# Kernel optimization log

Hardware: AMD Instinct MI355X
Metric: run time of the kernel (lower is better)

The kernel has to match this reference:

```python
import jax, jax.numpy as jnp
import numpy as np

N_RAYS = 4096
N_SAMPLES = 256
K = 12           # K_samples stochastic draws
GRID = 160       # world_size per axis
K0_DIM = 12
PE = 4           # viewbase_pe
WIDTH = 128
BG_LEN = 0.2
XYZ_MIN = -1.0 - BG_LEN
XYZ_MAX = 1.0 + BG_LEN
ALPHA_INIT = 1e-4
ACT_SHIFT = float(np.log(1.0 / (1.0 - ALPHA_INIT) - 1.0))
VOXEL_SIZE = (XYZ_MAX - XYZ_MIN) / GRID
STEPDIST = 0.5 * VOXEL_SIZE
INTERVAL = 0.5   # stepsize * voxel_size_ratio
NEAR = 0.1


def setup_inputs() -> dict:
    key = jax.random.key(0)
    ks = jax.random.split(key, 12)
    dim0 = 3 + 3 * PE * 2 + K0_DIM  # 39
    return {
        'rays_o': jax.random.normal(ks[0], (N_RAYS, 3)) * 0.1,
        'rays_d': jax.random.normal(ks[1], (N_RAYS, 3)),
        'density_grid': jax.random.normal(ks[2], (1, GRID, GRID, GRID)) * 0.1,
        'density_std_grid': jnp.ones((1, GRID, GRID, GRID)) + 0.01 * jax.random.normal(ks[3], (1, GRID, GRID, GRID)),
        'k0_grid': jax.random.normal(ks[4], (K0_DIM, GRID, GRID, GRID)) * 0.1,
        'w0': jax.random.normal(ks[5], (dim0, WIDTH)) / np.sqrt(dim0),
        'b0': jnp.zeros((WIDTH,)),
        'w1': jax.random.normal(ks[6], (WIDTH, WIDTH)) / np.sqrt(WIDTH),
        'b1': jnp.zeros((WIDTH,)),
        'w2': jax.random.normal(ks[7], (WIDTH, 6)) / np.sqrt(WIDTH),
        'b2': jnp.zeros((6,)),
        'eps_den': jax.random.normal(ks[8], (K,)),
        'eps_rgb': jax.random.normal(ks[9], (K, 3)),
    }


def trilinear(grid, pts):
    # grid: [C, X, Y, Z]; pts: [..., 3] in world coords [XYZ_MIN, XYZ_MAX]
    # align_corners=True style index mapping (as torch grid_sample in DVGO)
    u = (pts - XYZ_MIN) / (XYZ_MAX - XYZ_MIN) * (GRID - 1)
    i0 = jnp.clip(jnp.floor(u), 0, GRID - 2).astype(jnp.int32)
    f = u - i0.astype(u.dtype)
    x0, y0, z0 = i0[..., 0], i0[..., 1], i0[..., 2]
    x1, y1, z1 = x0 + 1, y0 + 1, z0 + 1
    fx, fy, fz = f[..., 0], f[..., 1], f[..., 2]
    gx, gy, gz = 1.0 - fx, 1.0 - fy, 1.0 - fz
    out = (grid[:, x0, y0, z0] * (gx * gy * gz)
         + grid[:, x1, y0, z0] * (fx * gy * gz)
         + grid[:, x0, y1, z0] * (gx * fy * gz)
         + grid[:, x0, y0, z1] * (gx * gy * fz)
         + grid[:, x1, y1, z0] * (fx * fy * gz)
         + grid[:, x1, y0, z1] * (fx * gy * fz)
         + grid[:, x0, y1, z1] * (gx * fy * fz)
         + grid[:, x1, y1, z1] * (fx * fy * fz))  # [C, ...]
    return jnp.moveaxis(out, 0, -1)


def _forward(rays_o, rays_d, density_grid, density_std_grid, k0_grid,
             w0, b0, w1, b1, w2, b2, eps_den, eps_rgb):
    viewdirs = rays_d / jnp.linalg.norm(rays_d, axis=-1, keepdims=True)  # [N,3]
    t = NEAR + STEPDIST * jnp.arange(N_SAMPLES, dtype=rays_o.dtype)      # [S]
    pts = rays_o[:, None, :] + viewdirs[:, None, :] * t[None, :, None]   # [N,S,3]

    # inf-norm scene contraction (contracted_norm='inf')
    norm = jnp.max(jnp.abs(pts), axis=-1, keepdims=True)
    inner = norm <= 1.0
    pts_c = jnp.where(inner, pts, pts / norm * ((1.0 + BG_LEN) - BG_LEN / norm))

    raw_den = trilinear(density_grid, pts_c)[..., 0]              # [N,S]
    raw_std = trilinear(density_std_grid, pts_c)[..., 0]          # [N,S]
    std = jax.nn.softplus(raw_std)
    # stochastic density draws: [N,S,K]
    den_k = raw_den[..., None] + std[..., None] * eps_den[None, None, :]
    alpha = 1.0 - jnp.exp(-jax.nn.softplus(den_k + ACT_SHIFT) * INTERVAL)
    # exclusive cumprod transmittance along samples
    T = jnp.cumprod(1.0 - alpha + 1e-10, axis=1)
    T = jnp.concatenate([jnp.ones_like(T[:, :1]), T[:, :-1]], axis=1)
    weights = alpha * T                                            # [N,S,K]

    # shading: k0 features + view PE -> rgbnet MLP -> 6 (rgb mean, rgb std)
    k0 = trilinear(k0_grid, pts_c)                                 # [N,S,12]
    freq = (2.0 ** jnp.arange(PE, dtype=pts.dtype))
    vd = viewdirs[:, :, None] * freq[None, None, :]                # [N,3,PE]
    vemb = jnp.concatenate([viewdirs, jnp.sin(vd).reshape(-1, 3 * PE),
                            jnp.cos(vd).reshape(-1, 3 * PE)], axis=-1)  # [N,27]
    feat = jnp.concatenate([k0, jnp.broadcast_to(vemb[:, None, :], (k0.shape[0], k0.shape[1], vemb.shape[-1]))], axis=-1)  # [N,S,39]
    h = jax.nn.relu(feat @ w0 + b0)
    h = jax.nn.relu(h @ w1 + b1)
    out6 = h @ w2 + b2                                             # [N,S,6]
    rgb_mean, rgb_raw_std = out6[..., :3], out6[..., 3:]
    rgb_std = jax.nn.softplus(rgb_raw_std)
    # stochastic rgb draws: [N,S,K,3]
    rgb_k = jax.nn.sigmoid(rgb_mean[:, :, None, :] + rgb_std[:, :, None, :] * eps_rgb[None, None, :, :])

    rgb_marched = jnp.sum(weights[..., None] * rgb_k, axis=1)      # [N,K,3]
    acc = jnp.sum(weights, axis=1)                                 # [N,K]
    rgb_marched = rgb_marched + (1.0 - acc)[..., None]             # white bg
    return jnp.mean(rgb_marched, axis=1)                           # [N,3]


def reference(rays_o, rays_d, density_grid, density_std_grid, k0_grid,
              w0, b0, w1, b1, w2, b2, eps_den, eps_rgb):
    return _forward(rays_o, rays_d, density_grid, density_std_grid, k0_grid,
                    w0, b0, w1, b1, w2, b2, eps_den, eps_rgb)
```

## Files before the change

kernel.cpp:

```cpp
#include <hip/hip_runtime.h>
#include <hip/hip_bf16.h>
#include <math.h>

#define NRAYS 4096
#define KK    12
#define GS    160
#define G3    (GS*GS*GS)
#define NSAMP (NRAYS*256)

typedef __bf16 bf16x8 __attribute__((ext_vector_type(8)));
typedef float  f32x4  __attribute__((ext_vector_type(4)));

#define W0KT_OFF 0
#define W1T_OFF  4096
#define W2T_OFF  20480
#define GRID_OFF_B 65536
#define FEAT_OFF_B 131137536UL
#define WKA_OFF_B  164691968UL
#define WKB_OFF_B  181469184UL
#define NEED_SPLIT 189857792UL
#define NEED_GRID  131137536UL

__device__ __forceinline__ float softplusf(float x) {
    return fmaxf(x, 0.f) + log1pf(expf(-fabsf(x)));
}
__device__ __forceinline__ float sigmoidf(float x) {
    return 1.f / (1.f + __expf(-x));
}
__device__ __forceinline__ unsigned pk2(float a, float b) {
    unsigned short x = __builtin_bit_cast(unsigned short, (__bf16)a);
    unsigned short y = __builtin_bit_cast(unsigned short, (__bf16)b);
    return (unsigned)x | ((unsigned)y << 16);
}
__device__ __forceinline__ float bfw(unsigned u, int hi) {
    return __builtin_bit_cast(float, hi ? (u & 0xffff0000u) : (u << 16));
}
__device__ __forceinline__ int xoff(int m, int kb) {
    return m * 256 + (kb ^ ((m & 7) << 4));
}

__global__ void prep_weights(const float* __restrict__ w0, const float* __restrict__ w1,
                             const float* __restrict__ w2, __bf16* __restrict__ ws)
{
    int i = blockIdx.x * 256 + threadIdx.x;
    if (i < 4096) {
        int n = i >> 5, k = i & 31;
        ws[W0KT_OFF + i] = (__bf16)((k < 12) ? w0[k * 128 + n] : 0.f);
    } else if (i < 20480) {
        int j = i - 4096;
        int n = j >> 7, k = j & 127;
        ws[W1T_OFF + j] = (__bf16)(w1[k * 128 + n]);
    } else if (i < 22528) {
        int j = i - 20480;
        int n = j >> 7, k = j & 127;
        ws[W2T_OFF + j] = (__bf16)((n < 6) ? w2[k * 6 + n] : 0.f);
    }
}

__global__ void prep_grid(const float* __restrict__ dg, const float* __restrict__ sg,
                          const float* __restrict__ k0, __bf16* __restrict__ dst)
{
    int v = blockIdx.x * 256 + threadIdx.x;
    float vals[16];
    vals[0] = dg[v];
    vals[1] = sg[v];
#pragma unroll
    for (int c = 0; c < 12; ++c) vals[2 + c] = k0[c * G3 + v];
    vals[14] = 0.f; vals[15] = 0.f;
    uint4 o0, o1;
    o0.x = pk2(vals[0],  vals[1]);  o0.y = pk2(vals[2],  vals[3]);
    o0.z = pk2(vals[4],  vals[5]);  o0.w = pk2(vals[6],  vals[7]);
    o1.x = pk2(vals[8],  vals[9]);  o1.y = pk2(vals[10], vals[11]);
    o1.z = pk2(vals[12], vals[13]); o1.w = pk2(vals[14], vals[15]);
    uint4* p = (uint4*)(dst + (size_t)v * 16);
    p[0] = o0; p[1] = o1;
}

__global__ __launch_bounds__(256, 2)
void voxgo_gather(const float* __restrict__ rays_o, const float* __restrict__ rays_d,
                  const char* __restrict__ gridb, const float* __restrict__ eps_den,
                  uint4* __restrict__ feat, uint4* __restrict__ wk_a,
                  uint2* __restrict__ wk_b)
{
    const float BGL   = 0.2f;
    const float XMIN  = -1.2f;
    const float SCALE = 159.0f / 2.4f;
    const float ACT_SHIFT = -9.2102403672f;
    const float STEP  = 0.0075f;
    const float NEART = 0.1f;

    __shared__ float scanw[4][KK];

    const int r    = blockIdx.x;
    const int s    = threadIdx.x;
    const int lane = s & 63;
    const int wv   = s >> 6;

    float dx = rays_d[r*3+0], dy = rays_d[r*3+1], dz = rays_d[r*3+2];
    float inv = rsqrtf(dx*dx + dy*dy + dz*dz);
    dx *= inv; dy *= inv; dz *= inv;
    float t  = NEART + STEP * (float)s;
    float px = rays_o[r*3+0] + dx*t;
    float py = rays_o[r*3+1] + dy*t;
    float pz = rays_o[r*3+2] + dz*t;
    float an = fmaxf(fabsf(px), fmaxf(fabsf(py), fabsf(pz)));
    if (an > 1.0f) {
        float sc = (1.0f + BGL - BGL/an) / an;
        px *= sc; py *= sc; pz *= sc;
    }
    float ux = (px - XMIN)*SCALE, uy = (py - XMIN)*SCALE, uz = (pz - XMIN)*SCALE;
    int ix = min(max((int)floorf(ux), 0), GS-2);
    int iy = min(max((int)floorf(uy), 0), GS-2);
    int iz = min(max((int)floorf(uz), 0), GS-2);
    float fx = ux-(float)ix, fy = uy-(float)iy, fz = uz-(float)iz;
    float gx = 1.f-fx, gy = 1.f-fy, gz = 1.f-fz;
    const int o000 = (ix*GS + iy)*GS + iz;
    float c00 = gx*gy, c01 = gx*fy, c10 = fx*gy, c11 = fx*fy;

    float acc14[14];
#pragma unroll
    for (int c = 0; c < 14; ++c) acc14[c] = 0.f;
    const int   vi[4] = { o000, o000 + GS, o000 + GS*GS, o000 + GS*GS + GS };
    const float cw[4] = { c00, c01, c10, c11 };
#pragma unroll
    for (int p = 0; p < 4; ++p) {
        const uint4* vp = (const uint4*)(gridb + (size_t)vi[p] * 32);
        uint4 q0 = vp[0], q1 = vp[1], q2 = vp[2], q3 = vp[3];
        float wz0 = cw[p]*gz, wz1 = cw[p]*fz;
        unsigned z0w[8] = { q0.x, q0.y, q0.z, q0.w, q1.x, q1.y, q1.z, q1.w };
        unsigned z1w[8] = { q2.x, q2.y, q2.z, q2.w, q3.x, q3.y, q3.z, q3.w };
#pragma unroll
        for (int c = 0; c < 14; ++c) {
            float a = bfw(z0w[c >> 1], c & 1);
            float b = bfw(z1w[c >> 1], c & 1);
            acc14[c] = fmaf(wz0, a, fmaf(wz1, b, acc14[c]));
        }
    }
    float raw_den = acc14[0];
    float raw_std = acc14[1];

    float stdv = softplusf(raw_std);
    float alpha[KK], incl[KK];
#pragma unroll
    for (int k = 0; k < KK; ++k) {
        float x  = raw_den + stdv * eps_den[k] + ACT_SHIFT;
        float a  = __expf(x) * 0.5f;
        float al = a - a*a*0.5f;
        alpha[k] = al;
        incl[k]  = 1.f - al + 1e-10f;
    }
#pragma unroll
    for (int d = 1; d < 64; d <<= 1) {
#pragma unroll
        for (int k = 0; k < KK; ++k) {
            float v = __shfl_up(incl[k], d, 64);
            if (lane >= d) incl[k] *= v;
        }
    }
    if (lane == 63) {
#pragma unroll
        for (int k = 0; k < KK; ++k) scanw[wv][k] = incl[k];
    }
    __syncthreads();
    float wk[KK];
#pragma unroll
    for (int k = 0; k < KK; ++k) {
        float pref = 1.f;
        for (int pw = 0; pw < wv; ++pw) pref *= scanw[pw][k];
        float ex = __shfl_up(incl[k], 1, 64);
        if (lane == 0) ex = 1.f;
        wk[k] = alpha[k] * (pref * ex);
    }

    const int rid = r * 256 + s;
    uint4 q0, q1;
    q0.x = pk2(acc14[2], acc14[3]);  q0.y = pk2(acc14[4],  acc14[5]);
    q0.z = pk2(acc14[6], acc14[7]);  q0.w = pk2(acc14[8],  acc14[9]);
    q1.x = pk2(acc14[10], acc14[11]); q1.y = pk2(acc14[12], acc14[13]);
    q1.z = 0u; q1.w = 0u;
    feat[(size_t)rid*2 + 0] = q0;
    feat[(size_t)rid*2 + 1] = q1;
    uint4 wa; uint2 wb;
    wa.x = pk2(wk[0], wk[1]); wa.y = pk2(wk[2], wk[3]);
    wa.z = pk2(wk[4], wk[5]); wa.w = pk2(wk[6], wk[7]);
    wb.x = pk2(wk[8], wk[9]); wb.y = pk2(wk[10], wk[11]);
    wk_a[rid] = wa;
    wk_b[rid] = wb;
}

__global__ __launch_bounds__(512, 2)
void voxgo_mlp(const float* __restrict__ rays_d,
               const float* __restrict__ w0, const float* __restrict__ b0,
               const float* __restrict__ b1, const float* __restrict__ b2,
               const float* __restrict__ eps_rgb,
               const __bf16* __restrict__ wsb,
               const uint4* __restrict__ feat, const uint4* __restrict__ wk_a,
               const uint2* __restrict__ wk_b,
               float* __restrict__ out)
{
    __shared__ char  xb[65536];
    __shared__ float h1ray[128];
    __shared__ float veb[27];
    __shared__ float red[8][3];

    const int r    = blockIdx.x;
    const int t    = threadIdx.x;
    const int lane = t & 63;
    const int wv   = t >> 6;
    const int lm = lane & 15, lk = lane >> 4;
    const int Mb = wv * 32;

    float dx = rays_d[r*3+0], dy = rays_d[r*3+1], dz = rays_d[r*3+2];
    float inv = rsqrtf(dx*dx + dy*dy + dz*dz);
    dx *= inv; dy *= inv; dz *= inv;
    if (t < 27) {
        float v;
        if (t < 3)       v = (t == 0) ? dx : (t == 1) ? dy : dz;
        else {
            int j = (t - 3) % 12;
            int a = j >> 2, p = j & 3;
            float arg = ((a == 0) ? dx : (a == 1) ? dy : dz) * (float)(1 << p);
            float sv, cv;
            __sincosf(arg, &sv, &cv);
            v = (t < 15) ? sv : cv;
        }
        veb[t] = v;
    }
    __syncthreads();
    if (t < 128) {
        float acc = b0[t];
#pragma unroll
        for (int j = 0; j < 27; ++j)
            acc = fmaf(veb[j], w0[(12 + j) * 128 + t], acc);
        h1ray[t] = acc;
    }
    __syncthreads();

    f32x4 acc[2][8];
#pragma unroll
    for (int nt = 0; nt < 8; ++nt) {
        f32x4 bi = *(const f32x4*)(h1ray + nt*16 + lk*4);
        acc[0][nt] = bi; acc[1][nt] = bi;
    }
    {
        const __bf16* w0t = wsb + W0KT_OFF;
        const uint4* fb = feat + (size_t)r * 512;
        bf16x8 bfr[2];
#pragma unroll
        for (int mt = 0; mt < 2; ++mt) {
            uint4 fq = {0u, 0u, 0u, 0u};
            if (lk < 2) fq = fb[(Mb + mt*16 + lm)*2 + lk];
            bfr[mt] = __builtin_bit_cast(bf16x8, fq);
        }
#pragma unroll
        for (int nt = 0; nt < 8; ++nt) {
            bf16x8 af = *(const bf16x8*)(w0t + (nt*16 + lm)*32 + lk*8);
#pragma unroll
            for (int mt = 0; mt < 2; ++mt)
                acc[mt][nt] = __builtin_amdgcn_mfma_f32_16x16x32_bf16(af, bfr[mt], acc[mt][nt], 0, 0, 0);
        }
    }
#pragma unroll
    for (int mt = 0; mt < 2; ++mt) {
        int mr = Mb + mt*16 + lm;
#pragma unroll
        for (int nt = 0; nt < 8; ++nt) {
            f32x4 v = acc[mt][nt];
            uint2 p;
            p.x = pk2(fmaxf(v.x, 0.f), fmaxf(v.y, 0.f));
            p.y = pk2(fmaxf(v.z, 0.f), fmaxf(v.w, 0.f));
            *(uint2*)(xb + xoff(mr, nt*32 + lk*8)) = p;
        }
    }
#pragma unroll
    for (int nt = 0; nt < 8; ++nt) {
        int n0 = nt*16 + lk*4;
        f32x4 bi = { b1[n0], b1[n0+1], b1[n0+2], b1[n0+3] };
        acc[0][nt] = bi; acc[1][nt] = bi;
    }
    {
        const __bf16* w1t = wsb + W1T_OFF;
#pragma unroll
        for (int ks = 0; ks < 4; ++ks) {
            bf16x8 bfr[2];
#pragma unroll
            for (int mt = 0; mt < 2; ++mt)
                bfr[mt] = *(const bf16x8*)(xb + xoff(Mb + mt*16 + lm, ks*64 + lk*16));
#pragma unroll
            for (int nt = 0; nt < 8; ++nt) {
                bf16x8 af = *(const bf16x8*)(w1t + (nt*16 + lm)*128 + ks*32 + lk*8);
#pragma unroll
                for (int mt = 0; mt < 2; ++mt)
                    acc[mt][nt] = __builtin_amdgcn_mfma_f32_16x16x32_bf16(af, bfr[mt], acc[mt][nt], 0, 0, 0);
            }
        }
    }
#pragma unroll
    for (int mt = 0; mt < 2; ++mt) {
        int mr = Mb + mt*16 + lm;
#pragma unroll
        for (int nt = 0; nt < 8; ++nt) {
            f32x4 v = acc[mt][nt];
            uint2 p;
            p.x = pk2(fmaxf(v.x, 0.f), fmaxf(v.y, 0.f));
            p.y = pk2(fmaxf(v.z, 0.f), fmaxf(v.w, 0.f));
            *(uint2*)(xb + xoff(mr, nt*32 + lk*8)) = p;
        }
    }
    f32x4 a3[2];
    {
        const __bf16* w2t = wsb + W2T_OFF;
        f32x4 bi;
        bi.x = (lk*4+0 < 6) ? b2[lk*4+0] : 0.f;
        bi.y = (lk*4+1 < 6) ? b2[lk*4+1] : 0.f;
        bi.z = (lk*4+2 < 6) ? b2[lk*4+2] : 0.f;
        bi.w = (lk*4+3 < 6) ? b2[lk*4+3] : 0.f;
        a3[0] = bi; a3[1] = bi;
#pragma unroll
        for (int ks = 0; ks < 4; ++ks) {
            bf16x8 af = *(const bf16x8*)(w2t + lm*128 + ks*32 + lk*8);
#pragma unroll
            for (int mt = 0; mt < 2; ++mt) {
                bf16x8 bfr = *(const bf16x8*)(xb + xoff(Mb + mt*16 + lm, ks*64 + lk*16));
                a3[mt] = __builtin_amdgcn_mfma_f32_16x16x32_bf16(af, bfr, a3[mt], 0, 0, 0);
            }
        }
    }
    {
        char* o6b = xb + wv * 8192;
#pragma unroll
        for (int mt = 0; mt < 2; ++mt)
            *(f32x4*)(o6b + (mt*16 + lm)*80 + lk*16) = a3[mt];
    }
    __syncthreads();

    float p0 = 0.f, p1 = 0.f, p2 = 0.f;
    {
        const int sm  = t & 255;
        const int hf  = t >> 8;
        const float* orow = (const float*)(xb + (sm >> 5) * 8192 + (sm & 31) * 80);
        float m0 = orow[0], m1 = orow[1], m2 = orow[2];
        float s0 = softplusf(orow[3]), s1 = softplusf(orow[4]), s2 = softplusf(orow[5]);
        const int rid = r * 256 + sm;
        uint4 wa = wk_a[rid];
        float w6[6];
        if (hf == 0) {
            w6[0] = bfw(wa.x, 0); w6[1] = bfw(wa.x, 1); w6[2] = bfw(wa.y, 0);
            w6[3] = bfw(wa.y, 1); w6[4] = bfw(wa.z, 0); w6[5] = bfw(wa.z, 1);
        } else {
            uint2 wb = wk_b[rid];
            w6[0] = bfw(wa.w, 0); w6[1] = bfw(wa.w, 1); w6[2] = bfw(wb.x, 0);
            w6[3] = bfw(wb.x, 1); w6[4] = bfw(wb.y, 0); w6[5] = bfw(wb.y, 1);
        }
        const int kb = hf * 6;
#pragma unroll
        for (int kk = 0; kk < 6; ++kk) {
            int k = kb + kk;
            float w = w6[kk];
            p0 += w * (sigmoidf(m0 + s0*eps_rgb[k*3+0]) - 1.f);
            p1 += w * (sigmoidf(m1 + s1*eps_rgb[k*3+1]) - 1.f);
            p2 += w * (sigmoidf(m2 + s2*eps_rgb[k*3+2]) - 1.f);
        }
    }
#pragma unroll
    for (int d = 32; d > 0; d >>= 1) {
        p0 += __shfl_down(p0, d, 64);
        p1 += __shfl_down(p1, d, 64);
        p2 += __shfl_down(p2, d, 64);
    }
    if (lane == 0) { red[wv][0] = p0; red[wv][1] = p1; red[wv][2] = p2; }
    __syncthreads();
    if (t == 0) {
        float a0 = 0.f, a1 = 0.f, a2 = 0.f;
#pragma unroll
        for (int w = 0; w < 8; ++w) { a0 += red[w][0]; a1 += red[w][1]; a2 += red[w][2]; }
        out[r*3+0] = 1.f + a0 * (1.f/12.f);
        out[r*3+1] = 1.f + a1 * (1.f/12.f);
        out[r*3+2] = 1.f + a2 * (1.f/12.f);
    }
}

template<int ITL>
__global__ __launch_bounds__(256, 2)
void voxgo_fwd(const float* __restrict__ rays_o, const float* __restrict__ rays_d,
               const float* __restrict__ dgrid, const float* __restrict__ sgrid,
               const float* __restrict__ k0g, const char* __restrict__ gridb,
               const float* __restrict__ w0, const float* __restrict__ b0,
               const float* __restrict__ b1, const float* __restrict__ b2,
               const float* __restrict__ eps_den, const float* __restrict__ eps_rgb,
               const __bf16* __restrict__ wsb,
               float* __restrict__ out)
{
    const float BGL   = 0.2f;
    const float XMIN  = -1.2f;
    const float SCALE = 159.0f / 2.4f;
    const float ACT_SHIFT = -9.2102403672f;
    const float STEP  = 0.0075f;
    const float NEART = 0.1f;

    __shared__ char  xb[65536];
    __shared__ float h1ray[128];
    __shared__ float veb[27];
    __shared__ float scanw[4][KK];
    __shared__ float red[4][3];

    const int r    = blockIdx.x;
    const int s    = threadIdx.x;
    const int lane = s & 63;
    const int wv   = s >> 6;
    const int lm = lane & 15, lk = lane >> 4;
    const int Mb = wv * 64;

    float dx = rays_d[r*3+0], dy = rays_d[r*3+1], dz = rays_d[r*3+2];
    float inv = rsqrtf(dx*dx + dy*dy + dz*dz);
    dx *= inv; dy *= inv; dz *= inv;
    if (s < 27) {
        float v;
        if (s < 3)       v = (s == 0) ? dx : (s == 1) ? dy : dz;
        else {
            int j = (s - 3) % 12;
            int a = j >> 2, p = j & 3;
            float arg = ((a == 0) ? dx : (a == 1) ? dy : dz) * (float)(1 << p);
            float sv, cv;
            __sincosf(arg, &sv, &cv);
            v = (s < 15) ? sv : cv;
        }
        veb[s] = v;
    }
    float t  = NEART + STEP * (float)s;
    float px = rays_o[r*3+0] + dx*t;
    float py = rays_o[r*3+1] + dy*t;
    float pz = rays_o[r*3+2] + dz*t;
    float an = fmaxf(fabsf(px), fmaxf(fabsf(py), fabsf(pz)));
    if (an > 1.0f) {
        float sc = (1.0f + BGL - BGL/an) / an;
        px *= sc; py *= sc; pz *= sc;
    }
    float ux = (px - XMIN)*SCALE, uy = (py - XMIN)*SCALE, uz = (pz - XMIN)*SCALE;
    int ix = min(max((int)floorf(ux), 0), GS-2);
    int iy = min(max((int)floorf(uy), 0), GS-2);
    int iz = min(max((int)floorf(uz), 0), GS-2);
    float fx = ux-(float)ix, fy = uy-(float)iy, fz = uz-(float)iz;
    float gx = 1.f-fx, gy = 1.f-fy, gz = 1.f-fz;
    const int o000 = (ix*GS + iy)*GS + iz;
    float c00 = gx*gy, c01 = gx*fy, c10 = fx*gy, c11 = fx*fy;

    float raw_den, raw_std, k0v[KK];
    if constexpr (ITL) {
        float acc14[14];
#pragma unroll
        for (int c = 0; c < 14; ++c) acc14[c] = 0.f;
        const int   vi[4] = { o000, o000 + GS, o000 + GS*GS, o000 + GS*GS + GS };
        const float cw[4] = { c00, c01, c10, c11 };
#pragma unroll
        for (int p = 0; p < 4; ++p) {
            const uint4* vp = (const uint4*)(gridb + (size_t)vi[p] * 32);
            uint4 q0 = vp[0], q1 = vp[1], q2 = vp[2], q3 = vp[3];
            float wz0 = cw[p]*gz, wz1 = cw[p]*fz;
            unsigned z0w[8] = { q0.x, q0.y, q0.z, q0.w, q1.x, q1.y, q1.z, q1.w };
            unsigned z1w[8] = { q2.x, q2.y, q2.z, q2.w, q3.x, q3.y, q3.z, q3.w };
#pragma unroll
            for (int c = 0; c < 14; ++c) {
                float a = bfw(z0w[c >> 1], c & 1);
                float b = bfw(z1w[c >> 1], c & 1);
                acc14[c] = fmaf(wz0, a, fmaf(wz1, b, acc14[c]));
            }
        }
        raw_den = acc14[0];
        raw_std = acc14[1];
#pragma unroll
        for (int c = 0; c < KK; ++c) k0v[c] = acc14[2 + c];
    } else {
        const int oY = GS, oX = GS*GS;
        auto tri = [&](const float* __restrict__ g) -> float {
            float v00 = g[o000]*gz       + g[o000+1]*fz;
            float v01 = g[o000+oY]*gz    + g[o000+oY+1]*fz;
            float v10 = g[o000+oX]*gz    + g[o000+oX+1]*fz;
            float v11 = g[o000+oX+oY]*gz + g[o000+oX+oY+1]*fz;
            return v00*c00 + v01*c01 + v10*c10 + v11*c11;
        };
        raw_den = tri(dgrid);
        raw_std = tri(sgrid);
#pragma unroll
        for (int c = 0; c < KK; ++c) k0v[c] = tri(k0g + c*G3);
    }

    float stdv = softplusf(raw_std);
    float alpha[KK], incl[KK];
#pragma unroll
    for (int k = 0; k < KK; ++k) {
        float x  = raw_den + stdv * eps_den[k] + ACT_SHIFT;
        float a  = __expf(x) * 0.5f;
        float al = a - a*a*0.5f;
        alpha[k] = al;
        incl[k]  = 1.f - al + 1e-10f;
    }
#pragma unroll
    for (int d = 1; d < 64; d <<= 1) {
#pragma unroll
        for (int k = 0; k < KK; ++k) {
            float v = __shfl_up(incl[k], d, 64);
            if (lane >= d) incl[k] *= v;
        }
    }
    if (lane == 63) {
#pragma unroll
        for (int k = 0; k < KK; ++k) scanw[wv][k] = incl[k];
    }
    {
        uint4 v;
        v.x = pk2(k0v[0], k0v[1]); v.y = pk2(k0v[2],  k0v[3]);
        v.z = pk2(k0v[4], k0v[5]); v.w = pk2(k0v[6],  k0v[7]);
        *(uint4*)(xb + xoff(s, 0)) = v;
        v.x = pk2(k0v[8], k0v[9]); v.y = pk2(k0v[10], k0v[11]);
        v.z = 0u; v.w = 0u;
        *(uint4*)(xb + xoff(s, 16)) = v;
        uint4 z4 = {0u, 0u, 0u, 0u};
        *(uint4*)(xb + xoff(s, 32)) = z4;
        *(uint4*)(xb + xoff(s, 48)) = z4;
    }
    __syncthreads();
    float wk[KK];
#pragma unroll
    for (int k = 0; k < KK; ++k) {
        float pref = 1.f;
        for (int pw = 0; pw < wv; ++pw) pref *= scanw[pw][k];
        float ex = __shfl_up(incl[k], 1, 64);
        if (lane == 0) ex = 1.f;
        wk[k] = alpha[k] * (pref * ex);
    }
    if (s < 128) {
        float acc = b0[s];
#pragma unroll
        for (int j = 0; j < 27; ++j)
            acc = fmaf(veb[j], w0[(12 + j) * 128 + s], acc);
        h1ray[s] = acc;
    }
    __syncthreads();

    f32x4 acc[4][8];
#pragma unroll
    for (int nt = 0; nt < 8; ++nt) {
        f32x4 bi = *(const f32x4*)(h1ray + nt*16 + lk*4);
#pragma unroll
        for (int mt = 0; mt < 4; ++mt) acc[mt][nt] = bi;
    }
    {
        const __bf16* w0t = wsb + W0KT_OFF;
        bf16x8 bfr[4];
#pragma unroll
        for (int mt = 0; mt < 4; ++mt)
            bfr[mt] = *(const bf16x8*)(xb + xoff(Mb + mt*16 + lm, lk*16));
#pragma unroll
        for (int nt = 0; nt < 8; ++nt) {
            bf16x8 af = *(const bf16x8*)(w0t + (nt*16 + lm)*32 + lk*8);
#pragma unroll
            for (int mt = 0; mt < 4; ++mt)
                acc[mt][nt] = __builtin_amdgcn_mfma_f32_16x16x32_bf16(af, bfr[mt], acc[mt][nt], 0, 0, 0);
        }
    }
#pragma unroll
    for (int mt = 0; mt < 4; ++mt) {
        int mr = Mb + mt*16 + lm;
#pragma unroll
        for (int nt = 0; nt < 8; ++nt) {
            f32x4 v = acc[mt][nt];
            uint2 p;
            p.x = pk2(fmaxf(v.x, 0.f), fmaxf(v.y, 0.f));
            p.y = pk2(fmaxf(v.z, 0.f), fmaxf(v.w, 0.f));
            *(uint2*)(xb + xoff(mr, nt*32 + lk*8)) = p;
        }
    }
#pragma unroll
    for (int nt = 0; nt < 8; ++nt) {
        int n0 = nt*16 + lk*4;
        f32x4 bi = { b1[n0], b1[n0+1], b1[n0+2], b1[n0+3] };
#pragma unroll
        for (int mt = 0; mt < 4; ++mt) acc[mt][nt] = bi;
    }
    {
        const __bf16* w1t = wsb + W1T_OFF;
#pragma unroll
        for (int ks = 0; ks < 4; ++ks) {
            bf16x8 bfr[4];
#pragma unroll
            for (int mt = 0; mt < 4; ++mt)
                bfr[mt] = *(const bf16x8*)(xb + xoff(Mb + mt*16 + lm, ks*64 + lk*16));
#pragma unroll
            for (int nt = 0; nt < 8; ++nt) {
                bf16x8 af = *(const bf16x8*)(w1t + (nt*16 + lm)*128 + ks*32 + lk*8);
#pragma unroll
                for (int mt = 0; mt < 4; ++mt)
                    acc[mt][nt] = __builtin_amdgcn_mfma_f32_16x16x32_bf16(af, bfr[mt], acc[mt][nt], 0, 0, 0);
            }
        }
    }
#pragma unroll
    for (int mt = 0; mt < 4; ++mt) {
        int mr = Mb + mt*16 + lm;
#pragma unroll
        for (int nt = 0; nt < 8; ++nt) {
            f32x4 v = acc[mt][nt];
            uint2 p;
            p.x = pk2(fmaxf(v.x, 0.f), fmaxf(v.y, 0.f));
            p.y = pk2(fmaxf(v.z, 0.f), fmaxf(v.w, 0.f));
            *(uint2*)(xb + xoff(mr, nt*32 + lk*8)) = p;
        }
    }
    f32x4 a3[4];
    {
        const __bf16* w2t = wsb + W2T_OFF;
        f32x4 bi;
        bi.x = (lk*4+0 < 6) ? b2[lk*4+0] : 0.f;
        bi.y = (lk*4+1 < 6) ? b2[lk*4+1] : 0.f;
        bi.z = (lk*4+2 < 6) ? b2[lk*4+2] : 0.f;
        bi.w = (lk*4+3 < 6) ? b2[lk*4+3] : 0.f;
#pragma unroll
        for (int mt = 0; mt < 4; ++mt) a3[mt] = bi;
#pragma unroll
        for (int ks = 0; ks < 4; ++ks) {
            bf16x8 af = *(const bf16x8*)(w2t + lm*128 + ks*32 + lk*8);
#pragma unroll
            for (int mt = 0; mt < 4; ++mt) {
                bf16x8 bfr = *(const bf16x8*)(xb + xoff(Mb + mt*16 + lm, ks*64 + lk*16));
                a3[mt] = __builtin_amdgcn_mfma_f32_16x16x32_bf16(af, bfr, a3[mt], 0, 0, 0);
            }
        }
    }
    {
        char* o6b = xb + wv * 16384;
#pragma unroll
        for (int mt = 0; mt < 4; ++mt)
            *(f32x4*)(o6b + (mt*16 + lm)*80 + lk*16) = a3[mt];
    }
    float p0 = 0.f, p1 = 0.f, p2 = 0.f;
    {
        const float* orow = (const float*)(xb + wv*16384 + lane*80);
        float m0 = orow[0], m1 = orow[1], m2 = orow[2];
        float s0 = softplusf(orow[3]), s1 = softplusf(orow[4]), s2 = softplusf(orow[5]);
#pragma unroll
        for (int k = 0; k < KK; ++k) {
            float w = wk[k];
            p0 += w * (sigmoidf(m0 + s0*eps_rgb[k*3+0]) - 1.f);
            p1 += w * (sigmoidf(m1 + s1*eps_rgb[k*3+1]) - 1.f);
            p2 += w * (sigmoidf(m2 + s2*eps_rgb[k*3+2]) - 1.f);
        }
    }
#pragma unroll
    for (int d = 32; d > 0; d >>= 1) {
        p0 += __shfl_down(p0, d, 64);
        p1 += __shfl_down(p1, d, 64);
        p2 += __shfl_down(p2, d, 64);
    }
    if (lane == 0) { red[wv][0] = p0; red[wv][1] = p1; red[wv][2] = p2; }
    __syncthreads();
    if (s == 0) {
        float a0 = red[0][0] + red[1][0] + red[2][0] + red[3][0];
        float a1 = red[0][1] + red[1][1] + red[2][1] + red[3][1];
        float a2 = red[0][2] + red[1][2] + red[2][2] + red[3][2];
        out[r*3+0] = 1.f + a0 * (1.f/12.f);
        out[r*3+1] = 1.f + a1 * (1.f/12.f);
        out[r*3+2] = 1.f + a2 * (1.f/12.f);
    }
}

extern "C" void kernel_launch(void* const* d_in, const int* in_sizes, int n_in,
                              void* d_out, int out_size, void* d_ws, size_t ws_size,
                              hipStream_t stream) {
    const float* rays_o  = (const float*)d_in[0];
    const float* rays_d  = (const float*)d_in[1];
    const float* dgrid   = (const float*)d_in[2];
    const float* sgrid   = (const float*)d_in[3];
    const float* k0g     = (const float*)d_in[4];
    const float* w0      = (const float*)d_in[5];
    const float* b0      = (const float*)d_in[6];
    const float* w1      = (const float*)d_in[7];
    const float* b1      = (const float*)d_in[8];
    const float* w2      = (const float*)d_in[9];
    const float* b2      = (const float*)d_in[10];
    const float* eps_den = (const float*)d_in[11];
    const float* eps_rgb = (const float*)d_in[12];
    float* out = (float*)d_out;
    __bf16* wsb = (__bf16*)d_ws;
    char*   base  = (char*)d_ws;
    char*   gridb = base + GRID_OFF_B;

    prep_weights<<<88, 256, 0, stream>>>(w0, w1, w2, wsb);
    if (ws_size >= NEED_SPLIT) {
        prep_grid<<<G3/256, 256, 0, stream>>>(dgrid, sgrid, k0g, (__bf16*)gridb);
        uint4* feat = (uint4*)(base + FEAT_OFF_B);
        uint4* wk_a = (uint4*)(base + WKA_OFF_B);
        uint2* wk_b = (uint2*)(base + WKB_OFF_B);
        voxgo_gather<<<NRAYS, 256, 0, stream>>>(rays_o, rays_d, gridb, eps_den,
                                                feat, wk_a, wk_b);
        voxgo_mlp<<<NRAYS, 512, 0, stream>>>(rays_d, w0, b0, b1, b2, eps_rgb,
                                             wsb, feat, wk_a, wk_b, out);
    } else if (ws_size >= NEED_GRID) {
        prep_grid<<<G3/256, 256, 0, stream>>>(dgrid, sgrid, k0g, (__bf16*)gridb);
        voxgo_fwd<1><<<NRAYS, 256, 0, stream>>>(rays_o, rays_d, dgrid, sgrid, k0g, gridb,
                                                w0, b0, b1, b2, eps_den, eps_rgb, wsb, out);
    } else {
        voxgo_fwd<0><<<NRAYS, 256, 0, stream>>>(rays_o, rays_d, dgrid, sgrid, k0g, gridb,
                                                w0, b0, b1, b2, eps_den, eps_rgb, wsb, out);
    }
}
```

Baseline: 299.4 us.

## Split MLP kernel into four 64-sample blocks per ray with LDS-staged weights

Result: slower. 323.6 us (+8.1%).

```diff
diff --git a/kernel.cpp b/kernel.cpp
--- a/kernel.cpp
+++ b/kernel.cpp
@@ -80,7 +80,7 @@
 void voxgo_gather(const float* __restrict__ rays_o, const float* __restrict__ rays_d,
                   const char* __restrict__ gridb, const float* __restrict__ eps_den,
                   uint4* __restrict__ feat, uint4* __restrict__ wk_a,
-                  uint2* __restrict__ wk_b)
+                  uint2* __restrict__ wk_b, float* __restrict__ out)
 {
     const float BGL   = 0.2f;
     const float XMIN  = -1.2f;
@@ -95,6 +95,8 @@
     const int s    = threadIdx.x;
     const int lane = s & 63;
     const int wv   = s >> 6;
+
+    if (s < 3) out[r*3 + s] = 1.0f;
 
     float dx = rays_d[r*3+0], dy = rays_d[r*3+1], dz = rays_d[r*3+2];
     float inv = rsqrtf(dx*dx + dy*dy + dz*dz);
@@ -188,7 +190,7 @@
     wk_b[rid] = wb;
 }
 
-__global__ __launch_bounds__(512, 2)
+__global__ __launch_bounds__(256, 2)
 void voxgo_mlp(const float* __restrict__ rays_d,
                const float* __restrict__ w0, const float* __restrict__ b0,
                const float* __restrict__ b1, const float* __restrict__ b2,
@@ -198,165 +200,152 @@
                const uint2* __restrict__ wk_b,
                float* __restrict__ out)
 {
-    __shared__ char  xb[65536];
-    __shared__ float h1ray[128];
-    __shared__ float veb[27];
-    __shared__ float red[8][3];
-
-    const int r    = blockIdx.x;
-    const int t    = threadIdx.x;
-    const int lane = t & 63;
-    const int wv   = t >> 6;
+    __shared__ char   wl[32768];
+    __shared__ __bf16 w0l[128*32];
+    __shared__ __bf16 w2l[16*128];
+    __shared__ char   act[64*256];
+    __shared__ float  h1ray[128];
+    __shared__ float  veb[32];
+    __shared__ float  red[4][4];
+
+    const int blk  = blockIdx.x;
+    const int r    = blk >> 2;
+    const int q    = blk & 3;
+    const int s    = threadIdx.x;
+    const int lane = s & 63;
+    const int wv   = s >> 6;
     const int lm = lane & 15, lk = lane >> 4;
-    const int Mb = wv * 32;
+    const int Mb = wv * 16;
+
+    {
+        const uint4* g1 = (const uint4*)(wsb + W1T_OFF);
+#pragma unroll
+        for (int j = 0; j < 8; ++j) {
+            int i = j * 256 + s;
+            *(uint4*)(wl + xoff(i >> 4, (i & 15) << 4)) = g1[i];
+        }
+        const uint4* g0 = (const uint4*)(wsb + W0KT_OFF);
+        ((uint4*)w0l)[s]       = g0[s];
+        ((uint4*)w0l)[s + 256] = g0[s + 256];
+        const uint4* g2 = (const uint4*)(wsb + W2T_OFF);
+        ((uint4*)w2l)[s] = g2[s];
+    }
 
     float dx = rays_d[r*3+0], dy = rays_d[r*3+1], dz = rays_d[r*3+2];
     float inv = rsqrtf(dx*dx + dy*dy + dz*dz);
     dx *= inv; dy *= inv; dz *= inv;
-    if (t < 27) {
+    if (s < 27) {
         float v;
-        if (t < 3)       v = (t == 0) ? dx : (t == 1) ? dy : dz;
+        if (s < 3)       v = (s == 0) ? dx : (s == 1) ? dy : dz;
         else {
-            int j = (t - 3) % 12;
+            int j = (s - 3) % 12;
             int a = j >> 2, p = j & 3;
             float arg = ((a == 0) ? dx : (a == 1) ? dy : dz) * (float)(1 << p);
             float sv, cv;
             __sincosf(arg, &sv, &cv);
-            v = (t < 15) ? sv : cv;
-        }
-        veb[t] = v;
-    }
-    __syncthreads();
-    if (t < 128) {
-        float acc = b0[t];
+            v = (s < 15) ? sv : cv;
+        }
+        veb[s] = v;
+    }
+
+    {
+        const int row  = s >> 2;
+        const int part = s & 3;
+        const size_t rid = (size_t)r * 256 + q * 64 + row;
+        uint4 v = {0u, 0u, 0u, 0u};
+        if (part < 2) v = feat[rid * 2 + part];
+        *(uint4*)(act + xoff(row, part * 16)) = v;
+    }
+    __syncthreads();
+
+    if (s < 128) {
+        float acc = b0[s];
 #pragma unroll
         for (int j = 0; j < 27; ++j)
-            acc = fmaf(veb[j], w0[(12 + j) * 128 + t], acc);
-        h1ray[t] = acc;
-    }
-    __syncthreads();
-
-    f32x4 acc[2][8];
+            acc = fmaf(veb[j], w0[(12 + j) * 128 + s], acc);
+        h1ray[s] = acc;
+    }
+    __syncthreads();
+
+    f32x4 acc[8];
+#pragma unroll
+    for (int nt = 0; nt < 8; ++nt)
+        acc[nt] = *(const f32x4*)(h1ray + nt*16 + lk*4);
+    {
+        bf16x8 bfr = *(const bf16x8*)(act + xoff(Mb + lm, lk*16));
+#pragma unroll
+        for (int nt = 0; nt < 8; ++nt) {
+            bf16x8 af = *(const bf16x8*)(w0l + (nt*16 + lm)*32 + lk*8);
+            acc[nt] = __builtin_amdgcn_mfma_f32_16x16x32_bf16(af, bfr, acc[nt], 0, 0, 0);
+        }
+    }
 #pragma unroll
     for (int nt = 0; nt < 8; ++nt) {
-        f32x4 bi = *(const f32x4*)(h1ray + nt*16 + lk*4);
-        acc[0][nt] = bi; acc[1][nt] = bi;
-    }
-    {
-        const __bf16* w0t = wsb + W0KT_OFF;
-        const uint4* fb = feat + (size_t)r * 512;
-        bf16x8 bfr[2];
-#pragma unroll
-        for (int mt = 0; mt < 2; ++mt) {
-            uint4 fq = {0u, 0u, 0u, 0u};
-            if (lk < 2) fq = fb[(Mb + mt*16 + lm)*2 + lk];
-            bfr[mt] = __builtin_bit_cast(bf16x8, fq);
-        }
-#pragma unroll
-        for (int nt = 0; nt < 8; ++nt) {
-            bf16x8 af = *(const bf16x8*)(w0t + (nt*16 + lm)*32 + lk*8);
-#pragma unroll
-            for (int mt = 0; mt < 2; ++mt)
-                acc[mt][nt] = __builtin_amdgcn_mfma_f32_16x16x32_bf16(af, bfr[mt], acc[mt][nt], 0, 0, 0);
-        }
-    }
-#pragma unroll
-    for (int mt = 0; mt < 2; ++mt) {
-        int mr = Mb + mt*16 + lm;
-#pragma unroll
-        for (int nt = 0; nt < 8; ++nt) {
-            f32x4 v = acc[mt][nt];
-            uint2 p;
-            p.x = pk2(fmaxf(v.x, 0.f), fmaxf(v.y, 0.f));
-            p.y = pk2(fmaxf(v.z, 0.f), fmaxf(v.w, 0.f));
-            *(uint2*)(xb + xoff(mr, nt*32 + lk*8)) = p;
-        }
+        f32x4 v = acc[nt];
+        uint2 p;
+        p.x = pk2(fmaxf(v.x, 0.f), fmaxf(v.y, 0.f));
+        p.y = pk2(fmaxf(v.z, 0.f), fmaxf(v.w, 0.f));
+        *(uint2*)(act + xoff(Mb + lm, nt*32 + lk*8)) = p;
     }
 #pragma unroll
     for (int nt = 0; nt < 8; ++nt) {
         int n0 = nt*16 + lk*4;
         f32x4 bi = { b1[n0], b1[n0+1], b1[n0+2], b1[n0+3] };
-        acc[0][nt] = bi; acc[1][nt] = bi;
-    }
-    {
-        const __bf16* w1t = wsb + W1T_OFF;
-#pragma unroll
-        for (int ks = 0; ks < 4; ++ks) {
-            bf16x8 bfr[2];
-#pragma unroll
-            for (int mt = 0; mt < 2; ++mt)
-                bfr[mt] = *(const bf16x8*)(xb + xoff(Mb + mt*16 + lm, ks*64 + lk*16));
-#pragma unroll
-            for (int nt = 0; nt < 8; ++nt) {
-                bf16x8 af = *(const bf16x8*)(w1t + (nt*16 + lm)*128 + ks*32 + lk*8);
-#pragma unroll
-                for (int mt = 0; mt < 2; ++mt)
-                    acc[mt][nt] = __builtin_amdgcn_mfma_f32_16x16x32_bf16(af, bfr[mt], acc[mt][nt], 0, 0, 0);
-            }
-        }
-    }
-#pragma unroll
-    for (int mt = 0; mt < 2; ++mt) {
-        int mr = Mb + mt*16 + lm;
+        acc[nt] = bi;
+    }
+#pragma unroll
+    for (int ks = 0; ks < 4; ++ks) {
+        bf16x8 bfr = *(const bf16x8*)(act + xoff(Mb + lm, ks*64 + lk*16));
 #pragma unroll
         for (int nt = 0; nt < 8; ++nt) {
-            f32x4 v = acc[mt][nt];
-            uint2 p;
-            p.x = pk2(fmaxf(v.x, 0.f), fmaxf(v.y, 0.f));
-            p.y = pk2(fmaxf(v.z, 0.f), fmaxf(v.w, 0.f));
-            *(uint2*)(xb + xoff(mr, nt*32 + lk*8)) = p;
-        }
-    }
-    f32x4 a3[2];
-    {
-        const __bf16* w2t = wsb + W2T_OFF;
-        f32x4 bi;
-        bi.x = (lk*4+0 < 6) ? b2[lk*4+0] : 0.f;
-        bi.y = (lk*4+1 < 6) ? b2[lk*4+1] : 0.f;
-        bi.z = (lk*4+2 < 6) ? b2[lk*4+2] : 0.f;
-        bi.w = (lk*4+3 < 6) ? b2[lk*4+3] : 0.f;
-        a3[0] = bi; a3[1] = bi;
-#pragma unroll
-        for (int ks = 0; ks < 4; ++ks) {
-            bf16x8 af = *(const bf16x8*)(w2t + lm*128 + ks*32 + lk*8);
-#pragma unroll
-            for (int mt = 0; mt < 2; ++mt) {
-                bf16x8 bfr = *(const bf16x8*)(xb + xoff(Mb + mt*16 + lm, ks*64 + lk*16));
-                a3[mt] = __builtin_amdgcn_mfma_f32_16x16x32_bf16(af, bfr, a3[mt], 0, 0, 0);
-            }
-        }
-    }
-    {
-        char* o6b = xb + wv * 8192;
-#pragma unroll
-        for (int mt = 0; mt < 2; ++mt)
-            *(f32x4*)(o6b + (mt*16 + lm)*80 + lk*16) = a3[mt];
-    }
+            bf16x8 af = *(const bf16x8*)(wl + xoff(nt*16 + lm, ks*64 + lk*16));
+            acc[nt] = __builtin_amdgcn_mfma_f32_16x16x32_bf16(af, bfr, acc[nt], 0, 0, 0);
+        }
+    }
+#pragma unroll
+    for (int nt = 0; nt < 8; ++nt) {
+        f32x4 v = acc[nt];
+        uint2 p;
+        p.x = pk2(fmaxf(v.x, 0.f), fmaxf(v.y, 0.f));
+        p.y = pk2(fmaxf(v.z, 0.f), fmaxf(v.w, 0.f));
+        *(uint2*)(act + xoff(Mb + lm, nt*32 + lk*8)) = p;
+    }
+    f32x4 a3;
+    a3.x = (lk*4+0 < 6) ? b2[lk*4+0] : 0.f;
+    a3.y = (lk*4+1 < 6) ? b2[lk*4+1] : 0.f;
+    a3.z = (lk*4+2 < 6) ? b2[lk*4+2] : 0.f;
+    a3.w = (lk*4+3 < 6) ? b2[lk*4+3] : 0.f;
+#pragma unroll
+    for (int ks = 0; ks < 4; ++ks) {
+        bf16x8 af  = *(const bf16x8*)(w2l + lm*128 + ks*32 + lk*8);
+        bf16x8 bfr = *(const bf16x8*)(act + xoff(Mb + lm, ks*64 + lk*16));
+        a3 = __builtin_amdgcn_mfma_f32_16x16x32_bf16(af, bfr, a3, 0, 0, 0);
+    }
+    *(f32x4*)(act + wv*4096 + lm*80 + lk*16) = a3;
     __syncthreads();
 
     float p0 = 0.f, p1 = 0.f, p2 = 0.f;
     {
-        const int sm  = t & 255;
-        const int hf  = t >> 8;
-        const float* orow = (const float*)(xb + (sm >> 5) * 8192 + (sm & 31) * 80);
+        const int row  = s & 63;
+        const int part = s >> 6;
+        const float* orow = (const float*)(act + (row >> 4)*4096 + (row & 15)*80);
         float m0 = orow[0], m1 = orow[1], m2 = orow[2];
         float s0 = softplusf(orow[3]), s1 = softplusf(orow[4]), s2 = softplusf(orow[5]);
-        const int rid = r * 256 + sm;
+        const size_t rid = (size_t)r * 256 + q * 64 + row;
         uint4 wa = wk_a[rid];
-        float w6[6];
-        if (hf == 0) {
-            w6[0] = bfw(wa.x, 0); w6[1] = bfw(wa.x, 1); w6[2] = bfw(wa.y, 0);
-            w6[3] = bfw(wa.y, 1); w6[4] = bfw(wa.z, 0); w6[5] = bfw(wa.z, 1);
-        } else {
-            uint2 wb = wk_b[rid];
-            w6[0] = bfw(wa.w, 0); w6[1] = bfw(wa.w, 1); w6[2] = bfw(wb.x, 0);
-            w6[3] = bfw(wb.x, 1); w6[4] = bfw(wb.y, 0); w6[5] = bfw(wb.y, 1);
-        }
-        const int kb = hf * 6;
-#pragma unroll
-        for (int kk = 0; kk < 6; ++kk) {
+        uint2 wb = wk_b[rid];
+        float wv0 = (part==0) ? bfw(wa.x,0) : (part==1) ? bfw(wa.y,1)
+                  : (part==2) ? bfw(wa.w,0) : bfw(wb.x,1);
+        float wv1 = (part==0) ? bfw(wa.x,1) : (part==1) ? bfw(wa.z,0)
+                  : (part==2) ? bfw(wa.w,1) : bfw(wb.y,0);
+        float wv2 = (part==0) ? bfw(wa.y,0) : (part==1) ? bfw(wa.z,1)
+                  : (part==2) ? bfw(wb.x,0) : bfw(wb.y,1);
+        float w3[3] = { wv0, wv1, wv2 };
+        const int kb = part * 3;
+#pragma unroll
+        for (int kk = 0; kk < 3; ++kk) {
             int k = kb + kk;
-            float w = w6[kk];
+            float w = w3[kk];
             p0 += w * (sigmoidf(m0 + s0*eps_rgb[k*3+0]) - 1.f);
             p1 += w * (sigmoidf(m1 + s1*eps_rgb[k*3+1]) - 1.f);
             p2 += w * (sigmoidf(m2 + s2*eps_rgb[k*3+2]) - 1.f);
@@ -370,13 +359,13 @@
     }
     if (lane == 0) { red[wv][0] = p0; red[wv][1] = p1; red[wv][2] = p2; }
     __syncthreads();
-    if (t == 0) {
-        float a0 = 0.f, a1 = 0.f, a2 = 0.f;
-#pragma unroll
-        for (int w = 0; w < 8; ++w) { a0 += red[w][0]; a1 += red[w][1]; a2 += red[w][2]; }
-        out[r*3+0] = 1.f + a0 * (1.f/12.f);
-        out[r*3+1] = 1.f + a1 * (1.f/12.f);
-        out[r*3+2] = 1.f + a2 * (1.f/12.f);
+    if (s == 0) {
+        float a0 = red[0][0] + red[1][0] + red[2][0] + red[3][0];
+        float a1 = red[0][1] + red[1][1] + red[2][1] + red[3][1];
+        float a2 = red[0][2] + red[1][2] + red[2][2] + red[3][2];
+        atomicAdd(&out[r*3+0], a0 * (1.f/12.f));
+        atomicAdd(&out[r*3+1], a1 * (1.f/12.f));
+        atomicAdd(&out[r*3+2], a2 * (1.f/12.f));
     }
 }
 
@@ -692,9 +681,9 @@
         uint4* wk_a = (uint4*)(base + WKA_OFF_B);
         uint2* wk_b = (uint2*)(base + WKB_OFF_B);
         voxgo_gather<<<NRAYS, 256, 0, stream>>>(rays_o, rays_d, gridb, eps_den,
-                                                feat, wk_a, wk_b);
-        voxgo_mlp<<<NRAYS, 512, 0, stream>>>(rays_d, w0, b0, b1, b2, eps_rgb,
-                                             wsb, feat, wk_a, wk_b, out);
+                                                feat, wk_a, wk_b, out);
+        voxgo_mlp<<<NRAYS*4, 256, 0, stream>>>(rays_d, w0, b0, b1, b2, eps_rgb,
+                                               wsb, feat, wk_a, wk_b, out);
     } else if (ws_size >= NEED_GRID) {
         prep_grid<<<G3/256, 256, 0, stream>>>(dgrid, sgrid, k0g, (__bf16*)gridb);
         voxgo_fwd<1><<<NRAYS, 256, 0, stream>>>(rays_o, rays_d, dgrid, sgrid, k0g, gridb,
```

## Split MLP kernel into half-ray blocks with LDS-staged features and atomic output

Applied to the files above, without the earlier changes.

Result: faster. 290.9 us (-2.9%).

```diff
diff --git a/kernel.cpp b/kernel.cpp
--- a/kernel.cpp
+++ b/kernel.cpp
@@ -22,7 +22,7 @@
 #define NEED_GRID  131137536UL
 
 __device__ __forceinline__ float softplusf(float x) {
-    return fmaxf(x, 0.f) + log1pf(expf(-fabsf(x)));
+    return fmaxf(x, 0.f) + __logf(1.f + __expf(-fabsf(x)));
 }
 __device__ __forceinline__ float sigmoidf(float x) {
     return 1.f / (1.f + __expf(-x));
@@ -80,7 +80,7 @@
 void voxgo_gather(const float* __restrict__ rays_o, const float* __restrict__ rays_d,
                   const char* __restrict__ gridb, const float* __restrict__ eps_den,
                   uint4* __restrict__ feat, uint4* __restrict__ wk_a,
-                  uint2* __restrict__ wk_b)
+                  uint2* __restrict__ wk_b, float* __restrict__ out)
 {
     const float BGL   = 0.2f;
     const float XMIN  = -1.2f;
@@ -95,6 +95,8 @@
     const int s    = threadIdx.x;
     const int lane = s & 63;
     const int wv   = s >> 6;
+
+    if (s < 3) out[r*3 + s] = 1.0f;
 
     float dx = rays_d[r*3+0], dy = rays_d[r*3+1], dz = rays_d[r*3+2];
     float inv = rsqrtf(dx*dx + dy*dy + dz*dz);
@@ -188,7 +190,7 @@
     wk_b[rid] = wb;
 }
 
-__global__ __launch_bounds__(512, 2)
+__global__ __launch_bounds__(256, 2)
 void voxgo_mlp(const float* __restrict__ rays_d,
                const float* __restrict__ w0, const float* __restrict__ b0,
                const float* __restrict__ b1, const float* __restrict__ b2,
@@ -198,41 +200,54 @@
                const uint2* __restrict__ wk_b,
                float* __restrict__ out)
 {
-    __shared__ char  xb[65536];
+    __shared__ char  act[128 * 256];
     __shared__ float h1ray[128];
-    __shared__ float veb[27];
-    __shared__ float red[8][3];
-
-    const int r    = blockIdx.x;
-    const int t    = threadIdx.x;
-    const int lane = t & 63;
-    const int wv   = t >> 6;
+    __shared__ float veb[32];
+    __shared__ float red[4][4];
+
+    const int blk  = blockIdx.x;
+    const int r    = blk >> 1;
+    const int hlf  = blk & 1;
+    const int s    = threadIdx.x;
+    const int lane = s & 63;
+    const int wv   = s >> 6;
     const int lm = lane & 15, lk = lane >> 4;
     const int Mb = wv * 32;
 
     float dx = rays_d[r*3+0], dy = rays_d[r*3+1], dz = rays_d[r*3+2];
     float inv = rsqrtf(dx*dx + dy*dy + dz*dz);
     dx *= inv; dy *= inv; dz *= inv;
-    if (t < 27) {
+    if (s < 27) {
         float v;
-        if (t < 3)       v = (t == 0) ? dx : (t == 1) ? dy : dz;
+        if (s < 3)       v = (s == 0) ? dx : (s == 1) ? dy : dz;
         else {
-            int j = (t - 3) % 12;
+            int j = (s - 3) % 12;
             int a = j >> 2, p = j & 3;
             float arg = ((a == 0) ? dx : (a == 1) ? dy : dz) * (float)(1 << p);
             float sv, cv;
             __sincosf(arg, &sv, &cv);
-            v = (t < 15) ? sv : cv;
-        }
-        veb[t] = v;
+            v = (s < 15) ? sv : cv;
+        }
+        veb[s] = v;
+    }
+
+    {
+        const int row  = s >> 1;
+        const int part = s & 1;
+        const size_t rid = (size_t)r * 256 + hlf * 128 + row;
+        uint4 v = feat[rid * 2 + part];
+        *(uint4*)(act + xoff(row, part * 16)) = v;
+        uint4 z4 = {0u, 0u, 0u, 0u};
+        *(uint4*)(act + xoff(row, 32 + part * 16)) = z4;
     }
     __syncthreads();
-    if (t < 128) {
-        float acc = b0[t];
+
+    if (s < 128) {
+        float acc = b0[s];
 #pragma unroll
         for (int j = 0; j < 27; ++j)
-            acc = fmaf(veb[j], w0[(12 + j) * 128 + t], acc);
-        h1ray[t] = acc;
+            acc = fmaf(veb[j], w0[(12 + j) * 128 + s], acc);
+        h1ray[s] = acc;
     }
     __syncthreads();
 
@@ -244,14 +259,10 @@
     }
     {
         const __bf16* w0t = wsb + W0KT_OFF;
-        const uint4* fb = feat + (size_t)r * 512;
         bf16x8 bfr[2];
 #pragma unroll
-        for (int mt = 0; mt < 2; ++mt) {
-            uint4 fq = {0u, 0u, 0u, 0u};
-            if (lk < 2) fq = fb[(Mb + mt*16 + lm)*2 + lk];
-            bfr[mt] = __builtin_bit_cast(bf16x8, fq);
-        }
+        for (int mt = 0; mt < 2; ++mt)
+            bfr[mt] = *(const bf16x8*)(act + xoff(Mb + mt*16 + lm, lk*16));
 #pragma unroll
         for (int nt = 0; nt < 8; ++nt) {
             bf16x8 af = *(const bf16x8*)(w0t + (nt*16 + lm)*32 + lk*8);
@@ -269,7 +280,7 @@
             uint2 p;
             p.x = pk2(fmaxf(v.x, 0.f), fmaxf(v.y, 0.f));
             p.y = pk2(fmaxf(v.z, 0.f), fmaxf(v.w, 0.f));
-            *(uint2*)(xb + xoff(mr, nt*32 + lk*8)) = p;
+            *(uint2*)(act + xoff(mr, nt*32 + lk*8)) = p;
         }
     }
 #pragma unroll
@@ -285,7 +296,7 @@
             bf16x8 bfr[2];
 #pragma unroll
             for (int mt = 0; mt < 2; ++mt)
-                bfr[mt] = *(const bf16x8*)(xb + xoff(Mb + mt*16 + lm, ks*64 + lk*16));
+                bfr[mt] = *(const bf16x8*)(act + xoff(Mb + mt*16 + lm, ks*64 + lk*16));
 #pragma unroll
             for (int nt = 0; nt < 8; ++nt) {
                 bf16x8 af = *(const bf16x8*)(w1t + (nt*16 + lm)*128 + ks*32 + lk*8);
@@ -304,7 +315,7 @@
             uint2 p;
             p.x = pk2(fmaxf(v.x, 0.f), fmaxf(v.y, 0.f));
             p.y = pk2(fmaxf(v.z, 0.f), fmaxf(v.w, 0.f));
-            *(uint2*)(xb + xoff(mr, nt*32 + lk*8)) = p;
+            *(uint2*)(act + xoff(mr, nt*32 + lk*8)) = p;
         }
     }
     f32x4 a3[2];
@@ -321,13 +332,13 @@
             bf16x8 af = *(const bf16x8*)(w2t + lm*128 + ks*32 + lk*8);
 #pragma unroll
             for (int mt = 0; mt < 2; ++mt) {
-                bf16x8 bfr = *(const bf16x8*)(xb + xoff(Mb + mt*16 + lm, ks*64 + lk*16));
+                bf16x8 bfr = *(const bf16x8*)(act + xoff(Mb + mt*16 + lm, ks*64 + lk*16));
                 a3[mt] = __builtin_amdgcn_mfma_f32_16x16x32_bf16(af, bfr, a3[mt], 0, 0, 0);
             }
         }
     }
     {
-        char* o6b = xb + wv * 8192;
+        char* o6b = act + wv * 8192;
 #pragma unroll
         for (int mt = 0; mt < 2; ++mt)
             *(f32x4*)(o6b + (mt*16 + lm)*80 + lk*16) = a3[mt];
@@ -336,12 +347,12 @@
 
     float p0 = 0.f, p1 = 0.f, p2 = 0.f;
     {
-        const int sm  = t & 255;
-        const int hf  = t >> 8;
-        const float* orow = (const float*)(xb + (sm >> 5) * 8192 + (sm & 31) * 80);
+        const int row = s & 127;
+        const int hf  = s >> 7;
+        const float* orow = (const float*)(act + (row >> 5)*8192 + (row & 31)*80);
         float m0 = orow[0], m1 = orow[1], m2 = orow[2];
         float s0 = softplusf(orow[3]), s1 = softplusf(orow[4]), s2 = softplusf(orow[5]);
-        const int rid = r * 256 + sm;
+        const size_t rid = (size_t)r * 256 + hlf * 128 + row;
         uint4 wa = wk_a[rid];
         float w6[6];
         if (hf == 0) {
@@ -370,13 +381,13 @@
     }
     if (lane == 0) { red[wv][0] = p0; red[wv][1] = p1; red[wv][2] = p2; }
     __syncthreads();
-    if (t == 0) {
-        float a0 = 0.f, a1 = 0.f, a2 = 0.f;
-#pragma unroll
-        for (int w = 0; w < 8; ++w) { a0 += red[w][0]; a1 += red[w][1]; a2 += red[w][2]; }
-        out[r*3+0] = 1.f + a0 * (1.f/12.f);
-        out[r*3+1] = 1.f + a1 * (1.f/12.f);
-        out[r*3+2] = 1.f + a2 * (1.f/12.f);
+    if (s == 0) {
+        float a0 = red[0][0] + red[1][0] + red[2][0] + red[3][0];
+        float a1 = red[0][1] + red[1][1] + red[2][1] + red[3][1];
+        float a2 = red[0][2] + red[1][2] + red[2][2] + red[3][2];
+        atomicAdd(&out[r*3+0], a0 * (1.f/12.f));
+        atomicAdd(&out[r*3+1], a1 * (1.f/12.f));
+        atomicAdd(&out[r*3+2], a2 * (1.f/12.f));
     }
 }
 
@@ -692,9 +703,9 @@
         uint4* wk_a = (uint4*)(base + WKA_OFF_B);
         uint2* wk_b = (uint2*)(base + WKB_OFF_B);
         voxgo_gather<<<NRAYS, 256, 0, stream>>>(rays_o, rays_d, gridb, eps_den,
-                                                feat, wk_a, wk_b);
-        voxgo_mlp<<<NRAYS, 512, 0, stream>>>(rays_d, w0, b0, b1, b2, eps_rgb,
-                                             wsb, feat, wk_a, wk_b, out);
+                                                feat, wk_a, wk_b, out);
+        voxgo_mlp<<<NRAYS*2, 256, 0, stream>>>(rays_d, w0, b0, b1, b2, eps_rgb,
+                                               wsb, feat, wk_a, wk_b, out);
     } else if (ws_size >= NEED_GRID) {
         prep_grid<<<G3/256, 256, 0, stream>>>(dgrid, sgrid, k0g, (__bf16*)gridb);
         voxgo_fwd<1><<<NRAYS, 256, 0, stream>>>(rays_o, rays_d, dgrid, sgrid, k0g, gridb,
```
